# Performance work log

Hardware: AMD Instinct MI355X
Metric: run time of the kernel (lower is better)

Reference implementation:

```python
import jax, jax.numpy as jnp
import numpy as np

N_NODES = 20000
DIM = 128
N_EDGES = 500000
BATCH = 16384
EPS = 1e-6  # torch.nn.PairwiseDistance default eps


def setup_inputs() -> dict:
    key = jax.random.key(0)
    k = jax.random.split(key, 8)
    edges = jax.random.randint(k[0], (2, N_EDGES), 0, N_NODES, dtype=jnp.int64 if jax.config.jax_enable_x64 else jnp.int32)
    nodes_p_star = jnp.sort(jax.random.randint(k[1], (BATCH,), 0, N_NODES))
    nodes_p = jnp.sort(jax.random.randint(k[2], (BATCH,), 0, N_NODES))
    # learned parameters, init in [-1, 1) as in the torch module
    beta_p = 2.0 * jax.random.uniform(k[3], (N_NODES,), dtype=jnp.float32) - 1.0
    beta_p_star = 2.0 * jax.random.uniform(k[4], (N_NODES,), dtype=jnp.float32) - 1.0
    p = 2.0 * jax.random.uniform(k[5], (N_NODES, DIM), dtype=jnp.float32) - 1.0
    p_star = 2.0 * jax.random.uniform(k[6], (N_NODES, DIM), dtype=jnp.float32) - 1.0
    return {
        "edges": edges,
        "nodes_p_star": nodes_p_star,
        "nodes_p": nodes_p,
        "beta_p": beta_p,
        "beta_p_star": beta_p_star,
        "p": p,
        "p_star": p_star,
    }


def reference(edges, nodes_p_star, nodes_p, beta_p, beta_p_star, p, p_star):
    # ---- link term: sum over observed edges of (beta - dist) ----
    beta_pair = beta_p_star[edges[0]] + beta_p[edges[1]]  # [E]
    diff = p[edges[0]] - p_star[edges[1]]                 # [E, D]
    # torch PairwiseDistance adds eps to the difference before the norm
    z_dist = jnp.sqrt(jnp.sum((diff + EPS) ** 2, axis=-1))
    link_term = jnp.sum(beta_pair - z_dist)

    # ---- non-link term: triu-masked sum of exp(beta - cdist) ----
    bps = beta_p_star[nodes_p_star]   # [Ns]
    bp = beta_p[nodes_p]              # [Np]
    ps = p_star[nodes_p_star]         # [Ns, D]
    pp = p[nodes_p]                   # [Np, D]
    beta_mat = bps[None, :] + bp[:, None]          # [Np, Ns]
    # cdist(ps, pp) -> [Ns, Np] via Gram trick
    sq = (jnp.sum(ps * ps, axis=-1)[:, None]
          + jnp.sum(pp * pp, axis=-1)[None, :]
          - 2.0 * jnp.einsum('nd,md->nm', ps, pp))
    dist_mat = jnp.sqrt(jnp.maximum(sq, 0.0))      # [Ns, Np]
    intensity = jnp.exp(beta_mat.T - dist_mat)     # [Ns, Np]
    non_link = jnp.sum(jnp.triu(intensity, k=1))

    return -(link_term - non_link)
```

## Files before the change

### kernel.cpp

```cpp
#include <hip/hip_runtime.h>
#include <hip/hip_bf16.h>

#define N_NODES 20000
#define DIM 128
#define N_EDGES 500000
#define BATCH 16384
#define EPS 1e-6f
#define L2E 1.4426950408889634f

typedef _Float16 half8 __attribute__((ext_vector_type(8)));
typedef _Float16 half4_t __attribute__((ext_vector_type(4)));
typedef float f32x4 __attribute__((ext_vector_type(4)));

__device__ __forceinline__ float fast_sqrtf(float x) {
#if __has_builtin(__builtin_amdgcn_sqrtf)
    return __builtin_amdgcn_sqrtf(x);
#else
    return sqrtf(x);
#endif
}
__device__ __forceinline__ float fast_exp2f(float x) {
#if __has_builtin(__builtin_amdgcn_exp2f)
    return __builtin_amdgcn_exp2f(x);
#else
    return exp2f(x);
#endif
}

#define NB_TILE 8256

#define OFF_PGEMM 0
#define OFF_PSH   33280
#define OFF_PPH   4227584
#define OFF_N2S   8421888
#define OFF_N2P   8487424
#define OFF_BPS   8552960
#define OFF_BP    8618496
#define OFF_P16   8684032
#define OFF_PS16  13804032
#define OFF_END   18924032

__global__ __launch_bounds__(256) void prep_kernel(
    const float* __restrict__ p, const float* __restrict__ p_star,
    const float* __restrict__ beta_p, const float* __restrict__ beta_ps,
    const int* __restrict__ nodes_ps, const int* __restrict__ nodes_p,
    _Float16* __restrict__ Ah, float* __restrict__ n2A, float* __restrict__ bA2,
    _Float16* __restrict__ Bh, float* __restrict__ n2B, float* __restrict__ bB2,
    _Float16* __restrict__ p16, _Float16* __restrict__ ps16)
{
    const int bx = blockIdx.x;
    const int g = threadIdx.x & 31;
    const int r8 = threadIdx.x >> 5;
    if (bx < 4096) {
        const bool isA = bx < 2048;
        int row = (isA ? bx : bx - 2048) * 8 + r8;
        int id = isA ? nodes_ps[row] : nodes_p[row];
        const float* src = isA ? p_star : p;
        float4 v = ((const float4*)(src + (size_t)id * DIM))[g];
        half4_t o;
        o[0] = (_Float16)v.x; o[1] = (_Float16)v.y; o[2] = (_Float16)v.z; o[3] = (_Float16)v.w;
        _Float16* dst = isA ? Ah : Bh;
        *(half4_t*)(dst + (size_t)row * DIM + g * 4) = o;
        float nrm = v.x * v.x + v.y * v.y + v.z * v.z + v.w * v.w;
        #pragma unroll
        for (int m = 16; m >= 1; m >>= 1) nrm += __shfl_xor(nrm, m, 32);
        if (g == 0) {
            if (isA) { n2A[row] = nrm; bA2[row] = L2E * beta_ps[id]; }
            else     { n2B[row] = nrm; bB2[row] = L2E * beta_p[id]; }
        }
    } else {
        const bool isP = bx < 6596;
        int row = (isP ? bx - 4096 : bx - 6596) * 8 + r8;
        const float* src = isP ? p : p_star;
        _Float16* dst = isP ? p16 : ps16;
        float4 v = ((const float4*)(src + (size_t)row * DIM))[g];
        half4_t o;
        o[0] = (_Float16)v.x; o[1] = (_Float16)v.y; o[2] = (_Float16)v.z; o[3] = (_Float16)v.w;
        *(half4_t*)(dst + (size_t)row * DIM + g * 4) = o;
    }
}

__global__ __launch_bounds__(512, 4) void main_kernel(
    const _Float16* __restrict__ Ag, const _Float16* __restrict__ Bg,
    const float* __restrict__ n2A, const float* __restrict__ n2B,
    const float* __restrict__ bA2, const float* __restrict__ bB2,
    const int* __restrict__ edges,
    const float* __restrict__ beta_p, const float* __restrict__ beta_ps,
    const _Float16* __restrict__ p16, const _Float16* __restrict__ ps16,
    const float* __restrict__ pf, const float* __restrict__ psf, int use16,
    float* __restrict__ pgemm)
{
    const int bx = blockIdx.x, by = blockIdx.y;
    int ti, tj;
    const int len = 128 - by;
    if (bx < len) { ti = by; tj = by + bx; }
    else          { ti = 127 - by; tj = 127 - (bx - len); }
    const int i0 = ti * 128, j0 = tj * 128;
    const int bid = by * 129 + bx;
    const bool diag = (ti == tj);

    __shared__ __align__(16) _Float16 As[128][136];
    __shared__ __align__(16) _Float16 Bs[128][136];
    __shared__ float smr[8];

    const int tid = threadIdx.x;
    const int lane = tid & 63;
    const int w = tid >> 6;
    const int wm = w & 3;
    const int wn = w >> 2;
    const int quad = lane >> 4;
    const int lr = lane & 15;

    float lsum = 0.f;
    half8 ea[2], eb[2];
    float ebeta[2] = {0.f, 0.f};
    bool ev[2];
    {
        #pragma unroll
        for (int t = 0; t < 2; ++t) {
            int e = bid * 64 + w * 8 + quad * 2 + t;
            ev[t] = (e < N_EDGES);
            if (ev[t]) {
                int e0 = edges[e];
                int e1 = edges[N_EDGES + e];
                if (use16) {
                    ea[t] = *(const half8*)(p16 + (size_t)e0 * DIM + lr * 8);
                    eb[t] = *(const half8*)(ps16 + (size_t)e1 * DIM + lr * 8);
                    if (lr == 0) ebeta[t] = beta_ps[e0] + beta_p[e1];
                } else {
                    const float* ar = pf + (size_t)e0 * DIM + lr * 8;
                    const float* br = psf + (size_t)e1 * DIM + lr * 8;
                    float s = 0.f;
                    #pragma unroll
                    for (int k = 0; k < 8; ++k) {
                        float d = ar[k] - br[k] + EPS;
                        s = fmaf(d, d, s);
                    }
                    #pragma unroll
                    for (int m = 8; m >= 1; m >>= 1) s += __shfl_xor(s, m, 16);
                    if (lr == 0) lsum -= (beta_ps[e0] + beta_p[e1]) - fast_sqrtf(s);
                }
            }
        }
    }

    const int ilo = i0 + wm * 32, jlo = j0 + wn * 64;
    float4 n2i[2], bi[2];
    #pragma unroll
    for (int mi = 0; mi < 2; ++mi) {
        n2i[mi] = *(const float4*)&n2A[ilo + mi * 16 + quad * 4];
        bi[mi]  = *(const float4*)&bA2[ilo + mi * 16 + quad * 4];
    }
    float n2j[4], bj[4];
    #pragma unroll
    for (int ni = 0; ni < 4; ++ni) {
        n2j[ni] = n2B[jlo + ni * 16 + lr];
        bj[ni]  = bB2[jlo + ni * 16 + lr];
    }

    #pragma unroll
    for (int c = tid; c < 2048; c += 512) {
        int row = c >> 4, col = (c & 15) * 8;
        *(uint4*)&As[row][col] = *(const uint4*)(Ag + (size_t)(i0 + row) * DIM + col);
        *(uint4*)&Bs[row][col] = *(const uint4*)(Bg + (size_t)(j0 + row) * DIM + col);
    }
    __syncthreads();

    int cls = 0;
    if (diag) cls = (wn == 0) ? (wm >= 2 ? 2 : 1) : (wm >= 2 ? 1 : 0);

    if (cls != 2) {
        f32x4 acc[2][4] = {};
        #pragma unroll
        for (int ks = 0; ks < 4; ++ks) {
            int koff = ks * 32 + quad * 8;
            half8 af[2], bf[4];
            #pragma unroll
            for (int u = 0; u < 2; ++u) af[u] = *(const half8*)&As[wm * 32 + u * 16 + lr][koff];
            #pragma unroll
            for (int v = 0; v < 4; ++v) bf[v] = *(const half8*)&Bs[wn * 64 + v * 16 + lr][koff];
            #pragma unroll
            for (int mi = 0; mi < 2; ++mi)
                #pragma unroll
                for (int ni = 0; ni < 4; ++ni)
                    acc[mi][ni] = __builtin_amdgcn_mfma_f32_16x16x32_f16(af[mi], bf[ni], acc[mi][ni], 0, 0, 0);
        }

        if (cls == 0) {
            #pragma unroll
            for (int mi = 0; mi < 2; ++mi)
                #pragma unroll
                for (int ni = 0; ni < 4; ++ni) {
                    f32x4 d = acc[mi][ni];
                    #pragma unroll
                    for (int r = 0; r < 4; ++r) {
                        float tt = ((const float*)&n2i[mi])[r] + n2j[ni];
                        float sq = fmaxf(fmaf(d[r], -2.f, tt), 0.f);
                        float arg = fmaf(fast_sqrtf(sq), -L2E, ((const float*)&bi[mi])[r] + bj[ni]);
                        lsum += fast_exp2f(arg);
                    }
                }
        } else {
            #pragma unroll
            for (int mi = 0; mi < 2; ++mi)
                #pragma unroll
                for (int ni = 0; ni < 4; ++ni) {
                    f32x4 d = acc[mi][ni];
                    #pragma unroll
                    for (int r = 0; r < 4; ++r) {
                        int ig = ilo + mi * 16 + quad * 4 + r;
                        int jg = jlo + ni * 16 + lr;
                        float tt = ((const float*)&n2i[mi])[r] + n2j[ni];
                        float sq = fmaxf(fmaf(d[r], -2.f, tt), 0.f);
                        float arg = fmaf(fast_sqrtf(sq), -L2E, ((const float*)&bi[mi])[r] + bj[ni]);
                        float ex = fast_exp2f(arg);
                        if (jg > ig) lsum += ex;
                    }
                }
        }
    }

    if (use16) {
        #pragma unroll
        for (int t = 0; t < 2; ++t) {
            if (ev[t]) {
                float s = 0.f;
                #pragma unroll
                for (int k = 0; k < 8; ++k) {
                    float d = (float)ea[t][k] - (float)eb[t][k] + EPS;
                    s = fmaf(d, d, s);
                }
                #pragma unroll
                for (int m = 8; m >= 1; m >>= 1) s += __shfl_xor(s, m, 16);
                if (lr == 0) lsum -= ebeta[t] - fast_sqrtf(s);
            }
        }
    }

    #pragma unroll
    for (int m = 32; m >= 1; m >>= 1) lsum += __shfl_xor(lsum, m, 64);
    if (lane == 0) smr[w] = lsum;
    __syncthreads();
    if (tid == 0) {
        float t = 0.f;
        #pragma unroll
        for (int i = 0; i < 8; ++i) t += smr[i];
        pgemm[bid] = t;
    }
}

__global__ __launch_bounds__(1024) void reduce_kernel(
    const float* __restrict__ pg, float* __restrict__ out)
{
    float s = 0.f;
    for (int k = threadIdx.x; k < NB_TILE; k += 1024) s += pg[k];
    #pragma unroll
    for (int m = 32; m >= 1; m >>= 1) s += __shfl_xor(s, m, 64);
    __shared__ float sm[16];
    if ((threadIdx.x & 63) == 0) sm[threadIdx.x >> 6] = s;
    __syncthreads();
    if (threadIdx.x == 0) {
        float t = 0.f;
        #pragma unroll
        for (int i = 0; i < 16; ++i) t += sm[i];
        out[0] = t;
    }
}

extern "C" void kernel_launch(void* const* d_in, const int* in_sizes, int n_in,
                              void* d_out, int out_size, void* d_ws, size_t ws_size,
                              hipStream_t stream) {
    const int* edges = (const int*)d_in[0];
    const int* nodes_p_star = (const int*)d_in[1];
    const int* nodes_p = (const int*)d_in[2];
    const float* beta_p = (const float*)d_in[3];
    const float* beta_p_star = (const float*)d_in[4];
    const float* p = (const float*)d_in[5];
    const float* p_star = (const float*)d_in[6];

    char* ws = (char*)d_ws;
    float* pgemm = (float*)(ws + OFF_PGEMM);
    _Float16* psh = (_Float16*)(ws + OFF_PSH);
    _Float16* pph = (_Float16*)(ws + OFF_PPH);
    float* n2s = (float*)(ws + OFF_N2S);
    float* n2p = (float*)(ws + OFF_N2P);
    float* bps2 = (float*)(ws + OFF_BPS);
    float* bp2 = (float*)(ws + OFF_BP);
    _Float16* p16 = (_Float16*)(ws + OFF_P16);
    _Float16* ps16 = (_Float16*)(ws + OFF_PS16);

    const int use16 = (ws_size >= (size_t)OFF_END) ? 1 : 0;

    prep_kernel<<<9096, 256, 0, stream>>>(
        p, p_star, beta_p, beta_p_star, nodes_p_star, nodes_p,
        psh, n2s, bps2, pph, n2p, bp2, p16, ps16);

    main_kernel<<<dim3(129, 64), 512, 0, stream>>>(
        psh, pph, n2s, n2p, bps2, bp2,
        edges, beta_p, beta_p_star, p16, ps16, p, p_star, use16,
        pgemm);

    reduce_kernel<<<1, 1024, 0, stream>>>(pgemm, (float*)d_out);
}
```

Measured before the change: 195.9 us.

## Stage GEMM tiles via direct global-to-LDS loads in two K halves, drop fp16 copies

The prep kernel no longer builds fp16 copies of the full p and p_star tables. Edge distances are now computed from fp32 rows, and their loads are issued up front and overlapped with tile staging. The GEMM operands are written pre-swizzled (XOR on 16-byte chunks) and staged into a 64-column LDS buffer with global_load_lds, in two K halves separated by barriers. LDS use is halved and launch bounds are raised to 8 blocks per CU for occupancy, at the cost of extra syncs and serialized staging between the halves.

```diff
diff --git a/kernel.cpp b/kernel.cpp
--- a/kernel.cpp
+++ b/kernel.cpp
@@ -1,5 +1,4 @@
 #include <hip/hip_runtime.h>
-#include <hip/hip_bf16.h>
 
 #define N_NODES 20000
 #define DIM 128
@@ -36,58 +35,85 @@
 #define OFF_N2P   8487424
 #define OFF_BPS   8552960
 #define OFF_BP    8618496
-#define OFF_P16   8684032
-#define OFF_PS16  13804032
-#define OFF_END   18924032
+#define OFF_END   8684032
 
 __global__ __launch_bounds__(256) void prep_kernel(
     const float* __restrict__ p, const float* __restrict__ p_star,
     const float* __restrict__ beta_p, const float* __restrict__ beta_ps,
     const int* __restrict__ nodes_ps, const int* __restrict__ nodes_p,
     _Float16* __restrict__ Ah, float* __restrict__ n2A, float* __restrict__ bA2,
-    _Float16* __restrict__ Bh, float* __restrict__ n2B, float* __restrict__ bB2,
-    _Float16* __restrict__ p16, _Float16* __restrict__ ps16)
+    _Float16* __restrict__ Bh, float* __restrict__ n2B, float* __restrict__ bB2)
 {
     const int bx = blockIdx.x;
     const int g = threadIdx.x & 31;
     const int r8 = threadIdx.x >> 5;
-    if (bx < 4096) {
-        const bool isA = bx < 2048;
-        int row = (isA ? bx : bx - 2048) * 8 + r8;
-        int id = isA ? nodes_ps[row] : nodes_p[row];
-        const float* src = isA ? p_star : p;
-        float4 v = ((const float4*)(src + (size_t)id * DIM))[g];
-        half4_t o;
-        o[0] = (_Float16)v.x; o[1] = (_Float16)v.y; o[2] = (_Float16)v.z; o[3] = (_Float16)v.w;
-        _Float16* dst = isA ? Ah : Bh;
-        *(half4_t*)(dst + (size_t)row * DIM + g * 4) = o;
-        float nrm = v.x * v.x + v.y * v.y + v.z * v.z + v.w * v.w;
-        #pragma unroll
-        for (int m = 16; m >= 1; m >>= 1) nrm += __shfl_xor(nrm, m, 32);
-        if (g == 0) {
-            if (isA) { n2A[row] = nrm; bA2[row] = L2E * beta_ps[id]; }
-            else     { n2B[row] = nrm; bB2[row] = L2E * beta_p[id]; }
-        }
-    } else {
-        const bool isP = bx < 6596;
-        int row = (isP ? bx - 4096 : bx - 6596) * 8 + r8;
-        const float* src = isP ? p : p_star;
-        _Float16* dst = isP ? p16 : ps16;
-        float4 v = ((const float4*)(src + (size_t)row * DIM))[g];
-        half4_t o;
-        o[0] = (_Float16)v.x; o[1] = (_Float16)v.y; o[2] = (_Float16)v.z; o[3] = (_Float16)v.w;
-        *(half4_t*)(dst + (size_t)row * DIM + g * 4) = o;
-    }
-}
-
-__global__ __launch_bounds__(512, 4) void main_kernel(
+    const bool isA = bx < 2048;
+    const int row = (isA ? bx : bx - 2048) * 8 + r8;
+    const int id = isA ? nodes_ps[row] : nodes_p[row];
+    const float* src = isA ? p_star : p;
+    float4 v = ((const float4*)(src + (size_t)id * DIM))[g];
+    half4_t o;
+    o[0] = (_Float16)v.x; o[1] = (_Float16)v.y; o[2] = (_Float16)v.z; o[3] = (_Float16)v.w;
+    const int h = g >> 4;
+    const int pc = ((g >> 1) & 7) ^ (row & 7);
+    _Float16* dst = isA ? Ah : Bh;
+    *(half4_t*)(dst + (size_t)row * DIM + (((h << 3) | pc) << 3) + (g & 1) * 4) = o;
+    float nrm = v.x * v.x + v.y * v.y + v.z * v.z + v.w * v.w;
+    #pragma unroll
+    for (int m = 16; m >= 1; m >>= 1) nrm += __shfl_xor(nrm, m, 32);
+    if (g == 0) {
+        if (isA) { n2A[row] = nrm; bA2[row] = L2E * beta_ps[id]; }
+        else     { n2B[row] = nrm; bB2[row] = L2E * beta_p[id]; }
+    }
+}
+
+#define STAGE(h)                                                                   \
+    {                                                                              \
+        _Pragma("unroll")                                                          \
+        for (int u = 0; u < 2; ++u) {                                              \
+            const int cidx = w * 128 + u * 64 + lane;                              \
+            const int row = cidx >> 3, cc = cidx & 7;                              \
+            const int ldsoff = (w * 128 + u * 64) * 16;                            \
+            __builtin_amdgcn_global_load_lds(                                      \
+                (const __attribute__((address_space(1))) void*)(gA +               \
+                    (((size_t)(i0 + row)) << 8) + ((h) << 7) + (cc << 4)),         \
+                (__attribute__((address_space(3))) void*)(ldsA + ldsoff), 16, 0, 0); \
+            __builtin_amdgcn_global_load_lds(                                      \
+                (const __attribute__((address_space(1))) void*)(gB +               \
+                    (((size_t)(j0 + row)) << 8) + ((h) << 7) + (cc << 4)),         \
+                (__attribute__((address_space(3))) void*)(ldsB + ldsoff), 16, 0, 0); \
+        }                                                                          \
+    }
+
+#define COMPUTE_HALF                                                               \
+    if (cls != 2) {                                                                \
+        _Pragma("unroll")                                                          \
+        for (int ks = 0; ks < 2; ++ks) {                                           \
+            const int lc = ks * 4 + quad;                                          \
+            const int pcx = (lc ^ k7) << 3;                                        \
+            half8 af[2], bf[4];                                                    \
+            _Pragma("unroll")                                                      \
+            for (int u = 0; u < 2; ++u)                                            \
+                af[u] = *(const half8*)&As[(wm * 32 + u * 16 + lr) * 64 + pcx];    \
+            _Pragma("unroll")                                                      \
+            for (int v = 0; v < 4; ++v)                                            \
+                bf[v] = *(const half8*)&Bs[(wn * 64 + v * 16 + lr) * 64 + pcx];    \
+            _Pragma("unroll")                                                      \
+            for (int mi = 0; mi < 2; ++mi)                                         \
+                _Pragma("unroll")                                                  \
+                for (int ni = 0; ni < 4; ++ni)                                     \
+                    acc[mi][ni] = __builtin_amdgcn_mfma_f32_16x16x32_f16(          \
+                        af[mi], bf[ni], acc[mi][ni], 0, 0, 0);                     \
+        }                                                                          \
+    }
+
+__global__ __launch_bounds__(512, 8) void main_kernel(
     const _Float16* __restrict__ Ag, const _Float16* __restrict__ Bg,
     const float* __restrict__ n2A, const float* __restrict__ n2B,
     const float* __restrict__ bA2, const float* __restrict__ bB2,
     const int* __restrict__ edges,
     const float* __restrict__ beta_p, const float* __restrict__ beta_ps,
-    const _Float16* __restrict__ p16, const _Float16* __restrict__ ps16,
-    const float* __restrict__ pf, const float* __restrict__ psf, int use16,
+    const float* __restrict__ pf, const float* __restrict__ psf,
     float* __restrict__ pgemm)
 {
     const int bx = blockIdx.x, by = blockIdx.y;
@@ -99,8 +125,8 @@
     const int bid = by * 129 + bx;
     const bool diag = (ti == tj);
 
-    __shared__ __align__(16) _Float16 As[128][136];
-    __shared__ __align__(16) _Float16 Bs[128][136];
+    __shared__ __align__(16) _Float16 As[128 * 64];
+    __shared__ __align__(16) _Float16 Bs[128 * 64];
     __shared__ float smr[8];
 
     const int tid = threadIdx.x;
@@ -110,80 +136,75 @@
     const int wn = w >> 2;
     const int quad = lane >> 4;
     const int lr = lane & 15;
+    const int k7 = lr & 7;
+
+    auto* ldsA = (__attribute__((address_space(3))) char*)As;
+    auto* ldsB = (__attribute__((address_space(3))) char*)Bs;
+    const auto* gA = (const __attribute__((address_space(1))) char*)Ag;
+    const auto* gB = (const __attribute__((address_space(1))) char*)Bg;
 
     float lsum = 0.f;
-    half8 ea[2], eb[2];
-    float ebeta[2] = {0.f, 0.f};
+    f32x4 la0[2], la1[2], lb0[2], lb1[2];
+    float eb2[2];
     bool ev[2];
-    {
-        #pragma unroll
-        for (int t = 0; t < 2; ++t) {
-            int e = bid * 64 + w * 8 + quad * 2 + t;
-            ev[t] = (e < N_EDGES);
-            if (ev[t]) {
-                int e0 = edges[e];
-                int e1 = edges[N_EDGES + e];
-                if (use16) {
-                    ea[t] = *(const half8*)(p16 + (size_t)e0 * DIM + lr * 8);
-                    eb[t] = *(const half8*)(ps16 + (size_t)e1 * DIM + lr * 8);
-                    if (lr == 0) ebeta[t] = beta_ps[e0] + beta_p[e1];
-                } else {
-                    const float* ar = pf + (size_t)e0 * DIM + lr * 8;
-                    const float* br = psf + (size_t)e1 * DIM + lr * 8;
-                    float s = 0.f;
-                    #pragma unroll
-                    for (int k = 0; k < 8; ++k) {
-                        float d = ar[k] - br[k] + EPS;
-                        s = fmaf(d, d, s);
-                    }
-                    #pragma unroll
-                    for (int m = 8; m >= 1; m >>= 1) s += __shfl_xor(s, m, 16);
-                    if (lr == 0) lsum -= (beta_ps[e0] + beta_p[e1]) - fast_sqrtf(s);
-                }
-            }
-        }
-    }
-
-    const int ilo = i0 + wm * 32, jlo = j0 + wn * 64;
-    float4 n2i[2], bi[2];
-    #pragma unroll
-    for (int mi = 0; mi < 2; ++mi) {
-        n2i[mi] = *(const float4*)&n2A[ilo + mi * 16 + quad * 4];
-        bi[mi]  = *(const float4*)&bA2[ilo + mi * 16 + quad * 4];
-    }
-    float n2j[4], bj[4];
-    #pragma unroll
-    for (int ni = 0; ni < 4; ++ni) {
-        n2j[ni] = n2B[jlo + ni * 16 + lr];
-        bj[ni]  = bB2[jlo + ni * 16 + lr];
-    }
-
-    #pragma unroll
-    for (int c = tid; c < 2048; c += 512) {
-        int row = c >> 4, col = (c & 15) * 8;
-        *(uint4*)&As[row][col] = *(const uint4*)(Ag + (size_t)(i0 + row) * DIM + col);
-        *(uint4*)&Bs[row][col] = *(const uint4*)(Bg + (size_t)(j0 + row) * DIM + col);
-    }
+    #pragma unroll
+    for (int t = 0; t < 2; ++t) {
+        int e = bid * 64 + w * 8 + quad * 2 + t;
+        ev[t] = (e < N_EDGES);
+        eb2[t] = 0.f;
+        if (ev[t]) {
+            int e0 = edges[e];
+            int e1 = edges[N_EDGES + e];
+            const float* ar = pf + (size_t)e0 * DIM + lr * 8;
+            const float* br = psf + (size_t)e1 * DIM + lr * 8;
+            la0[t] = *(const f32x4*)ar;       la1[t] = *(const f32x4*)(ar + 4);
+            lb0[t] = *(const f32x4*)br;       lb1[t] = *(const f32x4*)(br + 4);
+            if (lr == 0) eb2[t] = beta_ps[e0] + beta_p[e1];
+        }
+    }
+
+    STAGE(0)
+
+    #pragma unroll
+    for (int t = 0; t < 2; ++t) {
+        if (ev[t]) {
+            float s = 0.f;
+            #pragma unroll
+            for (int k = 0; k < 4; ++k) { float d = la0[t][k] - lb0[t][k] + EPS; s = fmaf(d, d, s); }
+            #pragma unroll
+            for (int k = 0; k < 4; ++k) { float d = la1[t][k] - lb1[t][k] + EPS; s = fmaf(d, d, s); }
+            #pragma unroll
+            for (int m = 8; m >= 1; m >>= 1) s += __shfl_xor(s, m, 16);
+            if (lr == 0) lsum -= eb2[t] - fast_sqrtf(s);
+        }
+    }
+
     __syncthreads();
 
     int cls = 0;
     if (diag) cls = (wn == 0) ? (wm >= 2 ? 2 : 1) : (wm >= 2 ? 1 : 0);
 
+    f32x4 acc[2][4] = {};
+
+    COMPUTE_HALF
+    __syncthreads();
+    STAGE(1)
+    __syncthreads();
+    COMPUTE_HALF
+
+    const int ilo = i0 + wm * 32, jlo = j0 + wn * 64;
     if (cls != 2) {
-        f32x4 acc[2][4] = {};
+        f32x4 n2i[2], bi[2];
         #pragma unroll
-        for (int ks = 0; ks < 4; ++ks) {
-            int koff = ks * 32 + quad * 8;
-            half8 af[2], bf[4];
-            #pragma unroll
-            for (int u = 0; u < 2; ++u) af[u] = *(const half8*)&As[wm * 32 + u * 16 + lr][koff];
-            #pragma unroll
-            for (int v = 0; v < 4; ++v) bf[v] = *(const half8*)&Bs[wn * 64 + v * 16 + lr][koff];
-            #pragma unroll
-            for (int mi = 0; mi < 2; ++mi)
-                #pragma unroll
-                for (int ni = 0; ni < 4; ++ni)
-                    acc[mi][ni] = __builtin_amdgcn_mfma_f32_16x16x32_f16(af[mi], bf[ni], acc[mi][ni], 0, 0, 0);
+        for (int mi = 0; mi < 2; ++mi) {
+            n2i[mi] = *(const f32x4*)&n2A[ilo + mi * 16 + quad * 4];
+            bi[mi]  = *(const f32x4*)&bA2[ilo + mi * 16 + quad * 4];
+        }
+        float n2j[4], bj[4];
+        #pragma unroll
+        for (int ni = 0; ni < 4; ++ni) {
+            n2j[ni] = n2B[jlo + ni * 16 + lr];
+            bj[ni]  = bB2[jlo + ni * 16 + lr];
         }
 
         if (cls == 0) {
@@ -194,9 +215,9 @@
                     f32x4 d = acc[mi][ni];
                     #pragma unroll
                     for (int r = 0; r < 4; ++r) {
-                        float tt = ((const float*)&n2i[mi])[r] + n2j[ni];
+                        float tt = n2i[mi][r] + n2j[ni];
                         float sq = fmaxf(fmaf(d[r], -2.f, tt), 0.f);
-                        float arg = fmaf(fast_sqrtf(sq), -L2E, ((const float*)&bi[mi])[r] + bj[ni]);
+                        float arg = fmaf(fast_sqrtf(sq), -L2E, bi[mi][r] + bj[ni]);
                         lsum += fast_exp2f(arg);
                     }
                 }
@@ -210,30 +231,13 @@
                     for (int r = 0; r < 4; ++r) {
                         int ig = ilo + mi * 16 + quad * 4 + r;
                         int jg = jlo + ni * 16 + lr;
-                        float tt = ((const float*)&n2i[mi])[r] + n2j[ni];
+                        float tt = n2i[mi][r] + n2j[ni];
                         float sq = fmaxf(fmaf(d[r], -2.f, tt), 0.f);
-                        float arg = fmaf(fast_sqrtf(sq), -L2E, ((const float*)&bi[mi])[r] + bj[ni]);
+                        float arg = fmaf(fast_sqrtf(sq), -L2E, bi[mi][r] + bj[ni]);
                         float ex = fast_exp2f(arg);
                         if (jg > ig) lsum += ex;
                     }
                 }
-        }
-    }
-
-    if (use16) {
-        #pragma unroll
-        for (int t = 0; t < 2; ++t) {
-            if (ev[t]) {
-                float s = 0.f;
-                #pragma unroll
-                for (int k = 0; k < 8; ++k) {
-                    float d = (float)ea[t][k] - (float)eb[t][k] + EPS;
-                    s = fmaf(d, d, s);
-                }
-                #pragma unroll
-                for (int m = 8; m >= 1; m >>= 1) s += __shfl_xor(s, m, 16);
-                if (lr == 0) lsum -= ebeta[t] - fast_sqrtf(s);
-            }
         }
     }
 
@@ -286,18 +290,14 @@
     float* n2p = (float*)(ws + OFF_N2P);
     float* bps2 = (float*)(ws + OFF_BPS);
     float* bp2 = (float*)(ws + OFF_BP);
-    _Float16* p16 = (_Float16*)(ws + OFF_P16);
-    _Float16* ps16 = (_Float16*)(ws + OFF_PS16);
-
-    const int use16 = (ws_size >= (size_t)OFF_END) ? 1 : 0;
-
-    prep_kernel<<<9096, 256, 0, stream>>>(
+
+    prep_kernel<<<4096, 256, 0, stream>>>(
         p, p_star, beta_p, beta_p_star, nodes_p_star, nodes_p,
-        psh, n2s, bps2, pph, n2p, bp2, p16, ps16);
+        psh, n2s, bps2, pph, n2p, bp2);
 
     main_kernel<<<dim3(129, 64), 512, 0, stream>>>(
         psh, pph, n2s, n2p, bps2, bp2,
-        edges, beta_p, beta_p_star, p16, ps16, p, p_star, use16,
+        edges, beta_p, beta_p_star, p, p_star,
         pgemm);
 
     reduce_kernel<<<1, 1024, 0, stream>>>(pgemm, (float*)d_out);
```

Result: slower. 487.2 us (+148.7%).
